# Performance work log

Hardware: AMD Instinct MI355X
Metric: run time of the kernel (lower is better)

## Reference

```python
import jax, jax.numpy as jnp
import numpy as np

L = 2048  # sequence length (number of atoms)
B = 8     # batch size


def setup_inputs() -> dict:
    key = jax.random.key(0)
    kx, ky, km = jax.random.split(key, 3)
    x = jax.random.normal(kx, (L, B, 3), dtype=jnp.float32) * 5.0
    y = jax.random.normal(ky, (L, B, 3), dtype=jnp.float32) * 5.0
    # mask values ARE indices (source: idx = mask[i][mask[i] != 0]).
    # Per-sample permutation of [0, L): exactly one zero entry per sample is
    # dropped by the mask!=0 filter, so every sample selects n = L-1 distinct rows.
    perms = jax.vmap(lambda k: jax.random.permutation(k, L))(jax.random.split(km, B))  # (B, L)
    mask = perms.T.astype(jnp.int32)  # (L, B)
    return {"x": x, "y": y, "mask": mask}


def _pair_dist(p):
    # p: (n, 3) -> (n, n) pairwise Euclidean distances
    sq = jnp.sum(p * p, axis=-1)                      # (n,)
    d = sq[:, None] + sq[None, :] - 2.0 * (p @ p.T)   # squared distances
    d = d - jnp.diag(jnp.diag(d))                     # exact-zero diagonal (as in source)
    d = jnp.maximum(d, 0.0)                           # relu
    pos = d > 0
    # safe sqrt: identical forward values, avoids nan grads at exact zeros
    return jnp.sqrt(jnp.where(pos, d, 1.0)) * pos


def reference(x, y, mask):
    xb = jnp.transpose(x, (1, 0, 2))  # (B, L, 3)
    yb = jnp.transpose(y, (1, 0, 2))
    mb = mask.T                        # (B, L)
    # drop the single zero per sample; order is irrelevant for dRMSD
    idx = jnp.sort(mb, axis=1)[:, 1:]  # (B, n) with n = L-1, distinct indices
    xs = jnp.take_along_axis(xb, idx[..., None], axis=1)  # (B, n, 3)
    ys = jnp.take_along_axis(yb, idx[..., None], axis=1)
    xd = jax.vmap(_pair_dist)(xs)      # (B, n, n)
    yd = jax.vmap(_pair_dist)(ys)
    D = yd - xd
    n = idx.shape[1]
    norms = jnp.sqrt(jnp.sum(D * D, axis=(1, 2)))          # per-sample Frobenius norm
    drmsd = jnp.sum(norms) / jnp.sqrt(jnp.float32(n * n - n)) / xb.shape[0]
    return drmsd.reshape(1)
```

## Files before the change

kernel.cpp:

```cpp
#include <hip/hip_runtime.h>
#include <math.h>

#define L 2048
#define B 8
#define N 2047
#define JC 64
#define II 4
#define BLOCK 256
#define ITILE (BLOCK * II)
#define NJC 32
#define NIT 2
#define NBLOCKS (NJC * NIT * B)

#if __has_builtin(__builtin_amdgcn_sqrtf)
#define FAST_SQRT(x) __builtin_amdgcn_sqrtf(x)
#else
#define FAST_SQRT(x) sqrtf(x)
#endif


__launch_bounds__(BLOCK)
__global__ void drmsd_kernel(const float* __restrict__ x, const float* __restrict__ y,
                             double* __restrict__ acc, unsigned int* __restrict__ ticket,
                             float* __restrict__ out) {
    __shared__ float4 ldsx[JC];
    __shared__ float4 ldsy[JC];

    const int jc  = blockIdx.x;
    const int it  = blockIdx.y;
    const int b   = blockIdx.z;
    const int tid = threadIdx.x;

    const int j0 = jc * JC;

    if (tid < JC) {
        int row = j0 + tid + 1;
        if (row > L - 1) row = L - 1;
        int base = (row * B + b) * 3;
        ldsx[tid] = make_float4(x[base], x[base + 1], x[base + 2], 0.f);
        ldsy[tid] = make_float4(y[base], y[base + 1], y[base + 2], 0.f);
    }
    __syncthreads();

    float xi0[II], xi1[II], xi2[II], yi0[II], yi1[II], yi2[II];
    float accf[II];
    int valid[II];
#pragma unroll
    for (int k = 0; k < II; ++k) {
        int i = it * ITILE + k * BLOCK + tid;
        valid[k] = (i < N);
        int row = i + 1;
        if (row > L - 1) row = L - 1;
        int base = (row * B + b) * 3;
        xi0[k] = x[base]; xi1[k] = x[base + 1]; xi2[k] = x[base + 2];
        yi0[k] = y[base]; yi1[k] = y[base + 1]; yi2[k] = y[base + 2];
        accf[k] = 0.f;
    }

    const int jmax = min(JC, N - j0);

    if (jmax == JC) {
#pragma unroll 4
        for (int jj = 0; jj < JC; ++jj) {
            float4 xj = ldsx[jj];
            float4 yj = ldsy[jj];
#pragma unroll
            for (int k = 0; k < II; ++k) {
                float dx0 = xi0[k] - xj.x, dx1 = xi1[k] - xj.y, dx2 = xi2[k] - xj.z;
                float dy0 = yi0[k] - yj.x, dy1 = yi1[k] - yj.y, dy2 = yi2[k] - yj.z;
                float dxs = dx0 * dx0 + dx1 * dx1 + dx2 * dx2;
                float dys = dy0 * dy0 + dy1 * dy1 + dy2 * dy2;
                float t = FAST_SQRT(dys) - FAST_SQRT(dxs);
                accf[k] += t * t;
            }
        }
    } else {
        for (int jj = 0; jj < jmax; ++jj) {
            float4 xj = ldsx[jj];
            float4 yj = ldsy[jj];
#pragma unroll
            for (int k = 0; k < II; ++k) {
                float dx0 = xi0[k] - xj.x, dx1 = xi1[k] - xj.y, dx2 = xi2[k] - xj.z;
                float dy0 = yi0[k] - yj.x, dy1 = yi1[k] - yj.y, dy2 = yi2[k] - yj.z;
                float dxs = dx0 * dx0 + dx1 * dx1 + dx2 * dx2;
                float dys = dy0 * dy0 + dy1 * dy1 + dy2 * dy2;
                float t = FAST_SQRT(dys) - FAST_SQRT(dxs);
                accf[k] += t * t;
            }
        }
    }

    float total = 0.f;
#pragma unroll
    for (int k = 0; k < II; ++k) total += valid[k] ? accf[k] : 0.f;

#pragma unroll
    for (int off = 32; off > 0; off >>= 1)
        total += __shfl_down(total, off, 64);

    __shared__ float wsum[BLOCK / 64];
    int lane = tid & 63, wv = tid >> 6;
    if (lane == 0) wsum[wv] = total;
    __syncthreads();

    if (tid == 0) {
        double s = (double)wsum[0] + (double)wsum[1] + (double)wsum[2] + (double)wsum[3];
        atomicAdd(&acc[b], s);
        __threadfence();
        unsigned int old = atomicAdd(ticket, 1u);
        if (old == NBLOCKS - 1) {
            double s2 = 0.0;
#pragma unroll
            for (int q = 0; q < B; ++q) s2 += sqrt(atomicAdd(&acc[q], 0.0));
            double denom = sqrt((double)N * (double)N - (double)N) * (double)B;
            out[0] = (float)(s2 / denom);
        }
    }
}

extern "C" void kernel_launch(void* const* d_in, const int* in_sizes, int n_in,
                              void* d_out, int out_size, void* d_ws, size_t ws_size,
                              hipStream_t stream) {
    const float* x = (const float*)d_in[0];
    const float* y = (const float*)d_in[1];
    float* out = (float*)d_out;

    double* acc = (double*)d_ws;
    unsigned int* ticket = (unsigned int*)((char*)d_ws + 64);

    hipMemsetAsync(d_ws, 0, 128, stream);

    dim3 grid(NJC, NIT, B);
    drmsd_kernel<<<grid, BLOCK, 0, stream>>>(x, y, acc, ticket, out);
}
```

Measured before the change: 83.97 us.

## Exploit pair symmetry with weighted upper-triangle tiles and drop workspace memset

Splits the i-range into four 512-row tiles and only processes j-chunks in the lower and diagonal part of the pair matrix, doubling the weight of off-diagonal tiles, since the squared distance difference is symmetric. This roughly halves the pairwise arithmetic. It also replaces per-sample atomic accumulation and the host memset with per-block partials in a static device array plus a modulo ticket counter, removing a separate memset launch. The final reduction is parallelised across threads in the last block; the weighting depends on the exact tile geometry being correct.

```diff
diff --git a/kernel.cpp b/kernel.cpp
--- a/kernel.cpp
+++ b/kernel.cpp
@@ -4,116 +4,119 @@
 #define L 2048
 #define B 8
 #define N 2047
+#define BLOCK 256
+#define II 2
+#define ITILE (BLOCK * II)
 #define JC 64
-#define II 4
-#define BLOCK 256
-#define ITILE (BLOCK * II)
-#define NJC 32
-#define NIT 2
-#define NBLOCKS (NJC * NIT * B)
+#define UNITS 80
+#define NBLOCKS (UNITS * B)
 
-#if __has_builtin(__builtin_amdgcn_sqrtf)
-#define FAST_SQRT(x) __builtin_amdgcn_sqrtf(x)
-#else
-#define FAST_SQRT(x) sqrtf(x)
-#endif
+__device__ double g_part[NBLOCKS];
+__device__ unsigned int g_ticket = 0;
 
+__device__ __forceinline__ float fsqrt_fast(float v) {
+    float r;
+    asm("v_sqrt_f32 %0, %1" : "=v"(r) : "v"(v));
+    return r;
+}
 
 __launch_bounds__(BLOCK)
 __global__ void drmsd_kernel(const float* __restrict__ x, const float* __restrict__ y,
-                             double* __restrict__ acc, unsigned int* __restrict__ ticket,
                              float* __restrict__ out) {
-    __shared__ float4 ldsx[JC];
-    __shared__ float4 ldsy[JC];
+    __shared__ float4 ldsx[JC], ldsy[JC];
+    __shared__ float wsum[BLOCK / 64];
+    __shared__ int amlast;
+    __shared__ double fsum8[B];
 
-    const int jc  = blockIdx.x;
-    const int it  = blockIdx.y;
-    const int b   = blockIdx.z;
+    const int bx  = blockIdx.x;
+    const int b   = blockIdx.y;
     const int tid = threadIdx.x;
 
-    const int j0 = jc * JC;
+    int ti, jc;
+    if (bx < 32)      { ti = 0; jc = bx;      }
+    else if (bx < 56) { ti = 1; jc = bx - 24; }
+    else if (bx < 72) { ti = 2; jc = bx - 40; }
+    else              { ti = 3; jc = bx - 48; }
 
     if (tid < JC) {
-        int row = j0 + tid + 1;
+        int row = jc * JC + tid + 1;
         if (row > L - 1) row = L - 1;
         int base = (row * B + b) * 3;
         ldsx[tid] = make_float4(x[base], x[base + 1], x[base + 2], 0.f);
         ldsy[tid] = make_float4(y[base], y[base + 1], y[base + 2], 0.f);
     }
+
+    float xi[II][3], yi[II][3], accf[II];
+    bool valid[II];
+#pragma unroll
+    for (int k = 0; k < II; ++k) {
+        int i = ti * ITILE + k * BLOCK + tid;
+        valid[k] = (i < N);
+        int row = i + 1; if (row > L - 1) row = L - 1;
+        int base = (row * B + b) * 3;
+        xi[k][0] = x[base]; xi[k][1] = x[base + 1]; xi[k][2] = x[base + 2];
+        yi[k][0] = y[base]; yi[k][1] = y[base + 1]; yi[k][2] = y[base + 2];
+        accf[k] = 0.f;
+    }
     __syncthreads();
 
-    float xi0[II], xi1[II], xi2[II], yi0[II], yi1[II], yi2[II];
-    float accf[II];
-    int valid[II];
+    const int jmax = min(JC, N - jc * JC);
+#pragma unroll 4
+    for (int jj = 0; jj < jmax; ++jj) {
+        float4 xj = ldsx[jj];
+        float4 yj = ldsy[jj];
 #pragma unroll
-    for (int k = 0; k < II; ++k) {
-        int i = it * ITILE + k * BLOCK + tid;
-        valid[k] = (i < N);
-        int row = i + 1;
-        if (row > L - 1) row = L - 1;
-        int base = (row * B + b) * 3;
-        xi0[k] = x[base]; xi1[k] = x[base + 1]; xi2[k] = x[base + 2];
-        yi0[k] = y[base]; yi1[k] = y[base + 1]; yi2[k] = y[base + 2];
-        accf[k] = 0.f;
-    }
-
-    const int jmax = min(JC, N - j0);
-
-    if (jmax == JC) {
-#pragma unroll 4
-        for (int jj = 0; jj < JC; ++jj) {
-            float4 xj = ldsx[jj];
-            float4 yj = ldsy[jj];
-#pragma unroll
-            for (int k = 0; k < II; ++k) {
-                float dx0 = xi0[k] - xj.x, dx1 = xi1[k] - xj.y, dx2 = xi2[k] - xj.z;
-                float dy0 = yi0[k] - yj.x, dy1 = yi1[k] - yj.y, dy2 = yi2[k] - yj.z;
-                float dxs = dx0 * dx0 + dx1 * dx1 + dx2 * dx2;
-                float dys = dy0 * dy0 + dy1 * dy1 + dy2 * dy2;
-                float t = FAST_SQRT(dys) - FAST_SQRT(dxs);
-                accf[k] += t * t;
-            }
-        }
-    } else {
-        for (int jj = 0; jj < jmax; ++jj) {
-            float4 xj = ldsx[jj];
-            float4 yj = ldsy[jj];
-#pragma unroll
-            for (int k = 0; k < II; ++k) {
-                float dx0 = xi0[k] - xj.x, dx1 = xi1[k] - xj.y, dx2 = xi2[k] - xj.z;
-                float dy0 = yi0[k] - yj.x, dy1 = yi1[k] - yj.y, dy2 = yi2[k] - yj.z;
-                float dxs = dx0 * dx0 + dx1 * dx1 + dx2 * dx2;
-                float dys = dy0 * dy0 + dy1 * dy1 + dy2 * dy2;
-                float t = FAST_SQRT(dys) - FAST_SQRT(dxs);
-                accf[k] += t * t;
-            }
+        for (int k = 0; k < II; ++k) {
+            float dx0 = xi[k][0] - xj.x, dx1 = xi[k][1] - xj.y, dx2 = xi[k][2] - xj.z;
+            float dy0 = yi[k][0] - yj.x, dy1 = yi[k][1] - yj.y, dy2 = yi[k][2] - yj.z;
+            float dxs = dx0 * dx0 + dx1 * dx1 + dx2 * dx2;
+            float dys = dy0 * dy0 + dy1 * dy1 + dy2 * dy2;
+            float t = fsqrt_fast(dys) - fsqrt_fast(dxs);
+            accf[k] += t * t;
         }
     }
 
-    float total = 0.f;
+    float tot = 0.f;
 #pragma unroll
-    for (int k = 0; k < II; ++k) total += valid[k] ? accf[k] : 0.f;
+    for (int k = 0; k < II; ++k) tot += valid[k] ? accf[k] : 0.f;
 
 #pragma unroll
     for (int off = 32; off > 0; off >>= 1)
-        total += __shfl_down(total, off, 64);
+        tot += __shfl_down(tot, off, 64);
 
-    __shared__ float wsum[BLOCK / 64];
     int lane = tid & 63, wv = tid >> 6;
-    if (lane == 0) wsum[wv] = total;
+    if (lane == 0) wsum[wv] = tot;
     __syncthreads();
 
     if (tid == 0) {
         double s = (double)wsum[0] + (double)wsum[1] + (double)wsum[2] + (double)wsum[3];
-        atomicAdd(&acc[b], s);
+        double w = (jc < 8 * (ti + 1)) ? 1.0 : 2.0;
+        g_part[b * UNITS + bx] = w * s;
         __threadfence();
-        unsigned int old = atomicAdd(ticket, 1u);
-        if (old == NBLOCKS - 1) {
-            double s2 = 0.0;
+        unsigned int old = atomicAdd(&g_ticket, 1u);
+        amlast = ((old % NBLOCKS) == NBLOCKS - 1) ? 1 : 0;
+    }
+    __syncthreads();
+
+    if (amlast) {
+        __threadfence();
+        int s8 = tid >> 5, g = tid & 31;
+        const double* p = g_part + s8 * UNITS;
+        double v = __hip_atomic_load(p + g,      __ATOMIC_RELAXED, __HIP_MEMORY_SCOPE_AGENT)
+                 + __hip_atomic_load(p + g + 32, __ATOMIC_RELAXED, __HIP_MEMORY_SCOPE_AGENT);
+        if (g < UNITS - 64)
+            v += __hip_atomic_load(p + g + 64, __ATOMIC_RELAXED, __HIP_MEMORY_SCOPE_AGENT);
 #pragma unroll
-            for (int q = 0; q < B; ++q) s2 += sqrt(atomicAdd(&acc[q], 0.0));
+        for (int off = 16; off > 0; off >>= 1)
+            v += __shfl_down(v, off, 32);
+        if (g == 0) fsum8[s8] = sqrt(v);
+        __syncthreads();
+        if (tid == 0) {
+            double t = 0.0;
+#pragma unroll
+            for (int q = 0; q < B; ++q) t += fsum8[q];
             double denom = sqrt((double)N * (double)N - (double)N) * (double)B;
-            out[0] = (float)(s2 / denom);
+            out[0] = (float)(t / denom);
         }
     }
 }
@@ -125,11 +128,6 @@
     const float* y = (const float*)d_in[1];
     float* out = (float*)d_out;
 
-    double* acc = (double*)d_ws;
-    unsigned int* ticket = (unsigned int*)((char*)d_ws + 64);
-
-    hipMemsetAsync(d_ws, 0, 128, stream);
-
-    dim3 grid(NJC, NIT, B);
-    drmsd_kernel<<<grid, BLOCK, 0, stream>>>(x, y, acc, ticket, out);
+    dim3 grid(UNITS, B);
+    drmsd_kernel<<<grid, BLOCK, 0, stream>>>(x, y, out);
 }
```

Result: faster. 80.44 us (-4.2%).
